# Kernel optimization log

Hardware: AMD Instinct MI355X
Metric: run time of the kernel (lower is better)

## Reference

```python
import jax, jax.numpy as jnp
import numpy as np

N_IN, N_OUT, N_TO = 64, 64, 16  # connection table: each output plane gets N_TO random input planes
K = N_OUT * N_TO                # 1024 connections
KH, KW = 3, 3
B, H, W = 4, 192, 192


def setup_inputs() -> dict:
    key = jax.random.key(0)
    kx, kw_, kb, kc = jax.random.split(key, 4)
    x = jax.random.normal(kx, (B, N_IN, H, W), dtype=jnp.float32)
    weight = jax.random.normal(kw_, (K, KH, KW), dtype=jnp.float32) * (1.0 / np.sqrt(KH * KW * N_TO))
    bias = jax.random.normal(kb, (N_OUT,), dtype=jnp.float32) * 0.01
    # maps.random semantics: each output plane j has exactly N_TO input connections
    conn_in = jax.random.randint(kc, (K,), 0, N_IN, dtype=jnp.int32)
    conn_out = jnp.repeat(jnp.arange(N_OUT, dtype=jnp.int32), N_TO)
    return {"x": x, "weight": weight, "bias": bias, "conn_in": conn_in, "conn_out": conn_out}


def reference(x, weight, bias, conn_in, conn_out):
    # x: [B, nIn, H, W]; weight: [K, kH, kW]; connection k convolves plane conn_in[k]
    # into plane conn_out[k] with its own kernel (valid conv, stride 1).
    nK = weight.shape[0]
    nOut = bias.shape[0]
    xg = x[:, conn_in]                       # [B, K, H, W] gather input planes per connection
    y = jax.lax.conv_general_dilated(
        xg, weight[:, None],                 # kernel [K, 1, kH, kW], grouped => per-connection conv
        window_strides=(1, 1), padding='VALID',
        feature_group_count=nK,
        dimension_numbers=('NCHW', 'OIHW', 'NCHW'))  # [B, K, Ho, Wo]
    # scatter-add connections into their output planes
    out = jax.ops.segment_sum(jnp.moveaxis(y, 1, 0), conn_out, num_segments=nOut)  # [nOut, B, Ho, Wo]
    return jnp.moveaxis(out, 0, 1) + bias[None, :, None, None]
```

## Files before the change

kernel.cpp:

```cpp
#include <hip/hip_runtime.h>
#include <hip/hip_bf16.h>

#define HH 192
#define WW 192
#define HOUT 190
#define NCH 64

typedef __attribute__((ext_vector_type(8))) short bf16x8;
typedef __attribute__((ext_vector_type(4))) float f32x4;

static __device__ __forceinline__ ushort f2bf(float f) {
    __hip_bfloat16 h = __float2bfloat16(f);
    return *reinterpret_cast<ushort*>(&h);
}
static __device__ __forceinline__ uint pack2bf(float lo, float hi) {
    return (uint)f2bf(lo) | ((uint)f2bf(hi) << 16);
}

__global__ __launch_bounds__(256) void build_w2(const float* __restrict__ w,
                                                const int* __restrict__ conn,
                                                ushort* __restrict__ w2l) {
    int idx = blockIdx.x * 256 + threadIdx.x;
    if (idx >= 4608) return;
    int o = idx / 72, rem = idx - o * 72, tap = rem >> 3, kc = rem & 7;
    int s = kc >> 2, g = kc & 3, wv = o >> 4, col = o & 15;
    ushort val[8];
    #pragma unroll
    for (int e = 0; e < 8; ++e) {
        int c = kc * 8 + e;
        float sum = 0.f;
        #pragma unroll
        for (int t = 0; t < 16; ++t) {
            int k = o * 16 + t;
            if (conn[k] == c) sum += w[k * 9 + tap];
        }
        val[e] = f2bf(sum);
    }
    uint4 v;
    v.x = (uint)val[0] | ((uint)val[1] << 16);
    v.y = (uint)val[2] | ((uint)val[3] << 16);
    v.z = (uint)val[4] | ((uint)val[5] << 16);
    v.w = (uint)val[6] | ((uint)val[7] << 16);
    size_t off = ((size_t)(tap * 2 + s)) * 2048 + wv * 512 + g * 128 + col * 8;
    *(uint4*)&w2l[off] = v;
}

__global__ __launch_bounds__(256, 3) void scm_mfma(
    const float* __restrict__ x,
    const ushort* __restrict__ w2l,
    const float* __restrict__ bias,
    float* __restrict__ out)
{
    __shared__ ushort xt[10 * 18 * 72];

    const int tid  = threadIdx.x;
    const int lane = tid & 63;
    const int wv   = tid >> 6;
    const int col  = lane & 15;
    const int g    = lane >> 4;

    const int bid = blockIdx.x;
    const int lid = (bid & 7) * 144 + (bid >> 3);
    const int b      = lid / 288;
    const int tileid = lid % 288;
    const int ti0 = (tileid / 12) * 8;
    const int tj0 = (tileid % 12) * 16;

    {
        const int srr  = lane / 18;
        const int scol = lane - srr * 18;
        const bool act = lane < 54;
        int gc = tj0 + scol; if (gc > 191) gc = 191;
        int gr0 = ti0 + srr;     if (gr0 > 191) gr0 = 191;
        int gr1 = ti0 + srr + 3; if (gr1 > 191) gr1 = 191;
        int gr2 = ti0 + srr + 6; if (gr2 > 191) gr2 = 191;
        int gr3 = ti0 + srr + 9; if (gr3 > 191) gr3 = 191;

        #pragma unroll
        for (int pass = 0; pass < 2; ++pass) {
            float v[8][4];
            #pragma unroll
            for (int pj = 0; pj < 8; ++pj) {
                const int c = wv * 16 + pass * 8 + pj;
                const float* xc = x + ((size_t)(b * NCH + c)) * (HH * WW);
                v[pj][0] = xc[gr0 * WW + gc];
                v[pj][1] = xc[gr1 * WW + gc];
                v[pj][2] = xc[gr2 * WW + gc];
                v[pj][3] = xc[gr3 * WW + gc];
            }
            __builtin_amdgcn_sched_barrier(0);
            if (act) {
                #pragma unroll
                for (int pp = 0; pp < 4; ++pp) {
                    const int c = wv * 16 + pass * 8 + 2 * pp;
                    uint k0 = pack2bf(v[2 * pp][0], v[2 * pp + 1][0]);
                    uint k1 = pack2bf(v[2 * pp][1], v[2 * pp + 1][1]);
                    uint k2 = pack2bf(v[2 * pp][2], v[2 * pp + 1][2]);
                    uint k3 = pack2bf(v[2 * pp][3], v[2 * pp + 1][3]);
                    *(uint*)&xt[((srr    ) * 18 + scol) * 72 + c] = k0;
                    *(uint*)&xt[((srr + 3) * 18 + scol) * 72 + c] = k1;
                    *(uint*)&xt[((srr + 6) * 18 + scol) * 72 + c] = k2;
                    if (srr == 0)
                        *(uint*)&xt[(9 * 18 + scol) * 72 + c] = k3;
                }
            }
        }
    }
    __syncthreads();

    f32x4 acc[8];
    #pragma unroll
    for (int i = 0; i < 8; ++i) acc[i] = (f32x4){0.f, 0.f, 0.f, 0.f};

    const ushort* ap0 = &xt[col * 72 + g * 8];
    const ushort* bpl = w2l + wv * 512 + g * 128 + col * 8;

    bf16x8 fA[10], fB[10];
    bf16x8 Bs[9];

#define LOADB(s) do {                                                          \
        _Pragma("unroll")                                                      \
        for (int _tap = 0; _tap < 9; ++_tap)                                   \
            Bs[_tap] = *(const bf16x8*)(bpl + (_tap * 2 + (s)) * 2048);        \
    } while (0)

#define LOADF(F, s, kw) do {                                                   \
        _Pragma("unroll")                                                      \
        for (int _R = 0; _R < 10; ++_R)                                        \
            F[_R] = *(const bf16x8*)(ap0 + (_R * 18 + (kw)) * 72 + (s) * 32);  \
    } while (0)

#define MFMA24(F, kw) do {                                                     \
        _Pragma("unroll")                                                      \
        for (int _Mt = 0; _Mt < 8; ++_Mt) {                                    \
            acc[_Mt] = __builtin_amdgcn_mfma_f32_16x16x32_bf16(Bs[kw],     F[_Mt],     acc[_Mt], 0, 0, 0); \
            acc[_Mt] = __builtin_amdgcn_mfma_f32_16x16x32_bf16(Bs[3+(kw)], F[_Mt + 1], acc[_Mt], 0, 0, 0); \
            acc[_Mt] = __builtin_amdgcn_mfma_f32_16x16x32_bf16(Bs[6+(kw)], F[_Mt + 2], acc[_Mt], 0, 0, 0); \
        }                                                                      \
    } while (0)

    LOADB(0);
    LOADF(fA, 0, 0);
    LOADF(fB, 0, 1);  MFMA24(fA, 0);
    LOADF(fA, 0, 2);  MFMA24(fB, 1);
    LOADF(fB, 1, 0);  MFMA24(fA, 2);
    LOADB(1);
    LOADF(fA, 1, 1);  MFMA24(fB, 0);
    LOADF(fB, 1, 2);  MFMA24(fA, 1);
    MFMA24(fB, 2);

#undef LOADB
#undef LOADF
#undef MFMA24

    const int pcol = tj0 + col;
    const int obase = 16 * wv + 4 * g;
    float bv[4];
    #pragma unroll
    for (int reg = 0; reg < 4; ++reg) bv[reg] = bias[obase + reg];

    if (pcol < HOUT) {
        #pragma unroll
        for (int Mt = 0; Mt < 8; ++Mt) {
            const int row = ti0 + Mt;
            if (row < HOUT) {
                float* rp = out + ((size_t)(b * NCH + obase) * HOUT + row) * HOUT + pcol;
                #pragma unroll
                for (int reg = 0; reg < 4; ++reg)
                    rp[(size_t)reg * HOUT * HOUT] = acc[Mt][reg] + bv[reg];
            }
        }
    }
}

extern "C" void kernel_launch(void* const* d_in, const int* in_sizes, int n_in,
                              void* d_out, int out_size, void* d_ws, size_t ws_size,
                              hipStream_t stream) {
    const float* x       = (const float*)d_in[0];
    const float* weight  = (const float*)d_in[1];
    const float* bias    = (const float*)d_in[2];
    const int*   conn_in = (const int*)d_in[3];

    ushort* w2l = (ushort*)d_ws;

    build_w2<<<dim3(18), dim3(256), 0, stream>>>(weight, conn_in, w2l);

    scm_mfma<<<dim3(1152), dim3(256), 0, stream>>>(x, w2l, bias, (float*)d_out);
}
```

Before: 32.77 us.

## Pre-cast input to bf16 channel-grouped layout and stage tiles via global_load_lds

Adds a separate pre-pass kernel that converts x to bf16 and rearranges it into a [B,H,8 channel groups,W,8] layout. The main kernel can then fill shared memory with direct global-to-LDS 16-byte loads instead of scalar fp32 loads followed by packing and LDS stores. This is meant to cut the main kernel's load and convert overhead and its halo re-reads of fp32 data. In exchange, the pre-pass adds a full read of x and a bf16 write and read through workspace, plus an extra launch.

```diff
diff --git a/kernel.cpp b/kernel.cpp
--- a/kernel.cpp
+++ b/kernel.cpp
@@ -5,16 +5,17 @@
 #define WW 192
 #define HOUT 190
 #define NCH 64
+#define XG_OFF 131072
 
 typedef __attribute__((ext_vector_type(8))) short bf16x8;
 typedef __attribute__((ext_vector_type(4))) float f32x4;
 
+typedef const __attribute__((address_space(1))) void gv_t;
+typedef __attribute__((address_space(3))) void lv_t;
+
 static __device__ __forceinline__ ushort f2bf(float f) {
     __hip_bfloat16 h = __float2bfloat16(f);
     return *reinterpret_cast<ushort*>(&h);
-}
-static __device__ __forceinline__ uint pack2bf(float lo, float hi) {
-    return (uint)f2bf(lo) | ((uint)f2bf(hi) << 16);
 }
 
 __global__ __launch_bounds__(256) void build_w2(const float* __restrict__ w,
@@ -45,17 +46,41 @@
     *(uint4*)&w2l[off] = v;
 }
 
+__global__ __launch_bounds__(256) void ksplit_cast(const float* __restrict__ x,
+                                                   ushort* __restrict__ xg) {
+    const int tid = threadIdx.x;
+    const int kg  = tid >> 5;
+    const int c0  = tid & 31;
+    const int r   = blockIdx.x / 6;
+    const int seg = blockIdx.x % 6;
+    const int b   = blockIdx.y;
+    const int col = seg * 32 + c0;
+
+    ushort t[8];
+    #pragma unroll
+    for (int k = 0; k < 8; ++k)
+        t[k] = f2bf(x[((size_t)(b * NCH + kg * 8 + k) * HH + r) * WW + col]);
+
+    uint4 v;
+    v.x = (uint)t[0] | ((uint)t[1] << 16);
+    v.y = (uint)t[2] | ((uint)t[3] << 16);
+    v.z = (uint)t[4] | ((uint)t[5] << 16);
+    v.w = (uint)t[6] | ((uint)t[7] << 16);
+    ushort* dst = xg + ((((size_t)b * HH + r) * 8 + kg) * WW + col) * 8;
+    *(uint4*)dst = v;
+}
+
 __global__ __launch_bounds__(256, 3) void scm_mfma(
-    const float* __restrict__ x,
+    const ushort* __restrict__ xg,
     const ushort* __restrict__ w2l,
     const float* __restrict__ bias,
     float* __restrict__ out)
 {
-    __shared__ ushort xt[10 * 18 * 72];
+    __shared__ ushort xt[1536 * 8];
 
     const int tid  = threadIdx.x;
+    const int wv   = tid >> 6;
     const int lane = tid & 63;
-    const int wv   = tid >> 6;
     const int col  = lane & 15;
     const int g    = lane >> 4;
 
@@ -66,57 +91,28 @@
     const int ti0 = (tileid / 12) * 8;
     const int tj0 = (tileid % 12) * 16;
 
-    {
-        const int srr  = lane / 18;
-        const int scol = lane - srr * 18;
-        const bool act = lane < 54;
-        int gc = tj0 + scol; if (gc > 191) gc = 191;
-        int gr0 = ti0 + srr;     if (gr0 > 191) gr0 = 191;
-        int gr1 = ti0 + srr + 3; if (gr1 > 191) gr1 = 191;
-        int gr2 = ti0 + srr + 6; if (gr2 > 191) gr2 = 191;
-        int gr3 = ti0 + srr + 9; if (gr3 > 191) gr3 = 191;
+    int goff[6];
+    #pragma unroll
+    for (int s = 0; s < 6; ++s) {
+        int u = s * 256 + tid;
+        int kg = u / 180;  int rem = u - kg * 180;
+        int row = rem / 18; int c = rem - row * 18;
+        if (kg > 7) { kg = 7; row = 9; c = 17; }
+        int gr = ti0 + row; if (gr > 191) gr = 191;
+        int gc = tj0 + c;   if (gc > 191) gc = 191;
+        goff[s] = ((((b * HH + gr) * 8 + kg) * WW + gc) * 8) * 2;
+    }
 
-        #pragma unroll
-        for (int pass = 0; pass < 2; ++pass) {
-            float v[8][4];
-            #pragma unroll
-            for (int pj = 0; pj < 8; ++pj) {
-                const int c = wv * 16 + pass * 8 + pj;
-                const float* xc = x + ((size_t)(b * NCH + c)) * (HH * WW);
-                v[pj][0] = xc[gr0 * WW + gc];
-                v[pj][1] = xc[gr1 * WW + gc];
-                v[pj][2] = xc[gr2 * WW + gc];
-                v[pj][3] = xc[gr3 * WW + gc];
-            }
-            __builtin_amdgcn_sched_barrier(0);
-            if (act) {
-                #pragma unroll
-                for (int pp = 0; pp < 4; ++pp) {
-                    const int c = wv * 16 + pass * 8 + 2 * pp;
-                    uint k0 = pack2bf(v[2 * pp][0], v[2 * pp + 1][0]);
-                    uint k1 = pack2bf(v[2 * pp][1], v[2 * pp + 1][1]);
-                    uint k2 = pack2bf(v[2 * pp][2], v[2 * pp + 1][2]);
-                    uint k3 = pack2bf(v[2 * pp][3], v[2 * pp + 1][3]);
-                    *(uint*)&xt[((srr    ) * 18 + scol) * 72 + c] = k0;
-                    *(uint*)&xt[((srr + 3) * 18 + scol) * 72 + c] = k1;
-                    *(uint*)&xt[((srr + 6) * 18 + scol) * 72 + c] = k2;
-                    if (srr == 0)
-                        *(uint*)&xt[(9 * 18 + scol) * 72 + c] = k3;
-                }
-            }
-        }
-    }
-    __syncthreads();
+    const char* xgb = (const char*)xg;
+    #pragma unroll
+    for (int s = 0; s < 6; ++s)
+        __builtin_amdgcn_global_load_lds((gv_t*)(xgb + goff[s]),
+                                         (lv_t*)((char*)xt + s * 4096 + wv * 1024),
+                                         16, 0, 0);
 
-    f32x4 acc[8];
-    #pragma unroll
-    for (int i = 0; i < 8; ++i) acc[i] = (f32x4){0.f, 0.f, 0.f, 0.f};
-
-    const ushort* ap0 = &xt[col * 72 + g * 8];
     const ushort* bpl = w2l + wv * 512 + g * 128 + col * 8;
-
+    bf16x8 Bs[9];
     bf16x8 fA[10], fB[10];
-    bf16x8 Bs[9];
 
 #define LOADB(s) do {                                                          \
         _Pragma("unroll")                                                      \
@@ -124,10 +120,20 @@
             Bs[_tap] = *(const bf16x8*)(bpl + (_tap * 2 + (s)) * 2048);        \
     } while (0)
 
+    LOADB(0);
+    asm volatile("s_waitcnt vmcnt(0)" ::: "memory");
+    __syncthreads();
+
+    f32x4 acc[8];
+    #pragma unroll
+    for (int i = 0; i < 8; ++i) acc[i] = (f32x4){0.f, 0.f, 0.f, 0.f};
+
+    const char* ap0 = (const char*)xt + (g * 180 + col) * 16;
+
 #define LOADF(F, s, kw) do {                                                   \
         _Pragma("unroll")                                                      \
         for (int _R = 0; _R < 10; ++_R)                                        \
-            F[_R] = *(const bf16x8*)(ap0 + (_R * 18 + (kw)) * 72 + (s) * 32);  \
+            F[_R] = *(const bf16x8*)(ap0 + (s) * 11520 + _R * 288 + (kw) * 16);\
     } while (0)
 
 #define MFMA24(F, kw) do {                                                     \
@@ -139,7 +145,6 @@
         }                                                                      \
     } while (0)
 
-    LOADB(0);
     LOADF(fA, 0, 0);
     LOADF(fB, 0, 1);  MFMA24(fA, 0);
     LOADF(fA, 0, 2);  MFMA24(fB, 1);
@@ -182,8 +187,10 @@
     const int*   conn_in = (const int*)d_in[3];
 
     ushort* w2l = (ushort*)d_ws;
+    ushort* xg  = (ushort*)((char*)d_ws + XG_OFF);
 
+    ksplit_cast<<<dim3(6 * HH, 4), dim3(256), 0, stream>>>(x, xg);
     build_w2<<<dim3(18), dim3(256), 0, stream>>>(weight, conn_in, w2l);
 
-    scm_mfma<<<dim3(1152), dim3(256), 0, stream>>>(x, w2l, bias, (float*)d_out);
+    scm_mfma<<<dim3(1152), dim3(256), 0, stream>>>(xg, w2l, bias, (float*)d_out);
 }
```

After: 38.85 us. +18.5%, slower.
